# Performance work log

Measured on AMD Instinct MI355X. Metric: run time of the kernel, lower is better.

## Reference

```python
import jax, jax.numpy as jnp
import numpy as np

FEAT = 128
N_RBF = 20
CUTOFF = 5.0
N_GRAPHS = 128
ATOMS = 64
N_ATOMS = N_GRAPHS * ATOMS  # 8192
N_EDGES = N_ATOMS * 32      # 262144


def setup_inputs() -> dict:
    key = jax.random.key(0)
    ks = jax.random.split(key, 12)
    s_j = jax.random.normal(ks[0], (N_ATOMS, FEAT), jnp.float32)
    v_j = jax.random.normal(ks[1], (N_ATOMS, FEAT, 3), jnp.float32)
    r_ij = jax.random.normal(ks[2], (N_EDGES, 3), jnp.float32) * 1.5
    nbrs = jax.random.randint(ks[3], (N_EDGES, 2), 0, N_ATOMS, dtype=jnp.int32)
    num_atoms = jnp.full((N_GRAPHS,), ATOMS, dtype=jnp.int32)
    sc = 0.05
    W1 = jax.random.normal(ks[4], (FEAT, FEAT), jnp.float32) * sc
    b1 = jnp.zeros((FEAT,), jnp.float32)
    W2 = jax.random.normal(ks[5], (FEAT, 3 * FEAT), jnp.float32) * sc
    b2 = jnp.zeros((3 * FEAT,), jnp.float32)
    Wr = jax.random.normal(ks[6], (N_RBF, 3 * FEAT), jnp.float32) * sc
    br = jnp.zeros((3 * FEAT,), jnp.float32)
    Wd = jax.random.normal(ks[7], (FEAT, 3 * FEAT), jnp.float32) * sc
    bd = jnp.zeros((3 * FEAT,), jnp.float32)
    return {"s_j": s_j, "v_j": v_j, "r_ij": r_ij, "nbrs": nbrs,
            "num_atoms": num_atoms, "W1": W1, "b1": b1, "W2": W2, "b2": b2,
            "Wr": Wr, "br": br, "Wd": Wd, "bd": bd}


def _forward(s_j, v_j, r_ij, nbrs, W1, b1, W2, b2, Wr, br, Wd, bd):
    # preprocess_r
    dist = jnp.linalg.norm(r_ij, axis=-1)            # [E]
    unit = r_ij / dist[:, None]                      # [E,3]

    # InvariantMessage: per-atom MLP, gather at nbrs[:,1], times radial filter
    phi = jax.nn.silu(s_j @ W1 + b1) @ W2 + b2       # [N, 3F]
    phi_e = phi[nbrs[:, 1]]                          # [E, 3F]
    n = jnp.arange(1, N_RBF + 1, dtype=jnp.float32)
    rbf = jnp.sin(n[None, :] * jnp.pi * dist[:, None] / CUTOFF) / dist[:, None]  # [E, n_rbf]
    env = jnp.where(dist < CUTOFF, 0.5 * (jnp.cos(jnp.pi * dist / CUTOFF) + 1.0), 0.0)
    w_s = (rbf @ Wr + br) * env[:, None]             # [E, 3F]
    inv_out = (phi_e * w_s).reshape(-1, 3, FEAT)     # [E, 3, F]

    split_0 = inv_out[:, 0, :][..., None]            # [E, F, 1]
    split_1 = inv_out[:, 1, :]                       # [E, F]
    split_2 = inv_out[:, 2, :][..., None]            # [E, F, 1]

    unit_add = split_2 * unit[:, None, :]            # [E, F, 3]
    delta_v_ij = unit_add + split_0 * v_j[nbrs[:, 1]]  # [E, F, 3]
    delta_s_ij = split_1                             # [E, F]

    seg = nbrs[:, 0]
    delta_v_i = jax.ops.segment_sum(delta_v_ij, seg, num_segments=N_ATOMS)
    delta_s_l = jax.ops.segment_sum(delta_s_ij, seg, num_segments=N_ATOMS)

    # NonLocalInteraction: per-graph exact softmax attention (uniform graph size)
    qkv = s_j @ Wd + bd                              # [N, 3F]
    Q, K, V = jnp.split(qkv, 3, axis=-1)
    Qb = Q.reshape(N_GRAPHS, ATOMS, FEAT)
    Kb = K.reshape(N_GRAPHS, ATOMS, FEAT)
    Vb = V.reshape(N_GRAPHS, ATOMS, FEAT)
    scores = jnp.einsum('bqf,bkf->bqk', Qb, Kb) / jnp.sqrt(jnp.float32(FEAT))
    att = jnp.einsum('bqk,bkf->bqf', jax.nn.softmax(scores, axis=-1), Vb)
    delta_s_nl = att.reshape(N_ATOMS, FEAT)

    delta_s_i = delta_s_l + delta_s_nl
    return delta_s_i, delta_v_i


def reference(s_j, v_j, r_ij, nbrs, num_atoms, W1, b1, W2, b2, Wr, br, Wd, bd):
    # num_atoms is uniform (ATOMS per graph); attention is batched accordingly.
    return _forward(s_j, v_j, r_ij, nbrs, W1, b1, W2, b2, Wr, br, Wd, bd)
```

## Files before the change

### kernel.cpp

```cpp
#include <hip/hip_runtime.h>
#include <hip/hip_bf16.h>
#include <cstdint>

#define FEAT    128
#define NRBF    20
#define NATOMS  8192
#define NEDGES  262144
#define NGRAPH  128
#define APG     64
#define PI_F    3.14159265358979323846f
#define CUTOFF_F 5.0f
#define QTUS    ((size_t)NATOMS * 32 * 6)

typedef unsigned int uint_t;
typedef unsigned short ushort_t;
typedef __attribute__((ext_vector_type(4))) float f32x4;
typedef __attribute__((ext_vector_type(4))) short short4v;
typedef __attribute__((ext_vector_type(8))) short short8;
struct U3 { uint_t x, y, z; };

__device__ __forceinline__ float bflo(uint_t u) { return __uint_as_float(u << 16); }
__device__ __forceinline__ float bfhi(uint_t u) { return __uint_as_float(u & 0xffff0000u); }
__device__ __forceinline__ float bfus(ushort_t u) { return __uint_as_float((uint_t)u << 16); }
__device__ __forceinline__ ushort_t f2bf(float f) {
  uint_t u = __float_as_uint(f);
  return (ushort_t)((u + 0x7fffu + ((u >> 16) & 1u)) >> 16);
}
__device__ __forceinline__ uint_t pack2(float lo, float hi) {
  return (uint_t)f2bf(lo) | ((uint_t)f2bf(hi) << 16);
}

__device__ __forceinline__ ushort_t swz_elem(const float* __restrict__ W, int N,
                                             int NT, int i) {
  int jj = i & 7, lane = (i >> 3) & 63, tile = i >> 9;
  int ks = tile / NT, ctg = tile - ks * NT;
  int g = lane >> 4, q = lane & 15;
  int k = 32 * ks + 4 * g + (jj & 3) + 16 * (jj >> 2);
  int c = 16 * ctg + q;
  return f2bf(W[(size_t)k * N + c]);
}

__global__ void prep_kernel(const float* __restrict__ v_j, const float* __restrict__ W1,
                            const float* __restrict__ W2, const float* __restrict__ Wd,
                            const float* __restrict__ Wr, const float* __restrict__ br,
                            ushort_t* __restrict__ PV, ushort_t* __restrict__ w1s,
                            ushort_t* __restrict__ w2s, ushort_t* __restrict__ wds,
                            ushort_t* __restrict__ wrs) {
  int i = blockIdx.x * 256 + threadIdx.x;
  if (i < NATOMS * FEAT) {
    int j = i >> 7, f = i & 127;
    int tbl = f >> 5, fl = f & 31;
    const float* vp = v_j + (size_t)i * 3;
    uint_t* o = reinterpret_cast<uint_t*>(PV + (size_t)tbl * QTUS + ((size_t)j * 32 + fl) * 6);
    o[0] = 0u;
    o[1] = pack2(0.f, vp[0]);
    o[2] = pack2(vp[1], vp[2]);
    return;
  }
  i -= NATOMS * FEAT;
  if (i < 16384) { w1s[i] = swz_elem(W1, 128, 8, i); return; }
  i -= 16384;
  if (i < 49152) { w2s[i] = swz_elem(W2, 384, 24, i); return; }
  i -= 49152;
  if (i < 49152) { wds[i] = swz_elem(Wd, 384, 24, i); return; }
  i -= 49152;
  if (i < 12288) {
    int jj = i & 7, lane = (i >> 3) & 63, ct = i >> 9;
    int g = lane >> 4, q = lane & 15;
    int k = 4 * g + (jj & 3) + 16 * (jj >> 2);
    int f = 16 * ct + q;
    float v = (k < NRBF) ? Wr[k * 384 + f] : (k == NRBF ? br[f] : 0.f);
    wrs[i] = f2bf(v);
  }
}

__global__ __launch_bounds__(256) void gemm_mfma(
    const void* __restrict__ Asrc, int a_f32, const ushort_t* __restrict__ Wswz,
    const float* __restrict__ bias, int N, int NT, int silu, int omode,
    void* __restrict__ p0, void* __restrict__ p1) {
  __shared__ ushort_t As[64][136];
  const int t = threadIdx.x;
  const int r0 = blockIdx.x * 64, c0 = blockIdx.y * 64;
  const int w = t >> 6, l = t & 63, g = l >> 4, q = l & 15;

  short8 bf[4][4];
  #pragma unroll
  for (int ks = 0; ks < 4; ++ks)
    #pragma unroll
    for (int ct = 0; ct < 4; ++ct)
      bf[ks][ct] = *reinterpret_cast<const short8*>(
          Wswz + ((size_t)(ks * NT + (c0 >> 4) + ct) * 64 + l) * 8);

  if (a_f32) {
    const float* Af = (const float*)Asrc;
    for (int i = t; i < 64 * 32; i += 256) {
      int r = i >> 5, k4 = i & 31;
      float4 v = *reinterpret_cast<const float4*>(Af + (size_t)(r0 + r) * 128 + 4 * k4);
      ushort4 o = {f2bf(v.x), f2bf(v.y), f2bf(v.z), f2bf(v.w)};
      *reinterpret_cast<ushort4*>(&As[r][4 * k4]) = o;
    }
  } else {
    const ushort_t* Ab = (const ushort_t*)Asrc;
    for (int i = t; i < 64 * 16; i += 256) {
      int r = i >> 4, g8 = i & 15;
      short8 v = *reinterpret_cast<const short8*>(Ab + (size_t)(r0 + r) * 128 + 8 * g8);
      *reinterpret_cast<short8*>(&As[r][8 * g8]) = v;
    }
  }
  __syncthreads();

  f32x4 acc[4] = {};
  #pragma unroll
  for (int ks = 0; ks < 4; ++ks) {
    const ushort_t* ap = &As[16 * w + q][32 * ks + 4 * g];
    short4v alo = *reinterpret_cast<const short4v*>(ap);
    short4v ahi = *reinterpret_cast<const short4v*>(ap + 16);
    short8 af;
    af[0] = alo[0]; af[1] = alo[1]; af[2] = alo[2]; af[3] = alo[3];
    af[4] = ahi[0]; af[5] = ahi[1]; af[6] = ahi[2]; af[7] = ahi[3];
    #pragma unroll
    for (int ct = 0; ct < 4; ++ct)
      acc[ct] = __builtin_amdgcn_mfma_f32_16x16x32_bf16(af, bf[ks][ct], acc[ct], 0, 0, 0);
  }

  #pragma unroll
  for (int ct = 0; ct < 4; ++ct) {
    int col = c0 + 16 * ct + q;
    float bb = bias[col];
    #pragma unroll
    for (int r = 0; r < 4; ++r) {
      float o = acc[ct][r] + bb;
      if (silu) o = o / (1.f + __expf(-o));
      int row = r0 + 16 * w + 4 * g + r;
      if (omode == 1) {
        ((ushort_t*)p0)[(size_t)row * N + col] = f2bf(o);
      } else if (omode == 2) {
        int f = col & 127, s = col >> 7;
        int tbl = f >> 5, fl = f & 31;
        ((ushort_t*)p0)[(size_t)tbl * QTUS + ((size_t)row * 32 + fl) * 6 + s] = f2bf(o);
      } else {
        if (col < 128) ((float*)p0)[(size_t)row * 128 + col] = o;
        else           ((ushort_t*)p1)[(size_t)row * 256 + col - 128] = f2bf(o);
      }
    }
  }
}

__global__ void hist_kernel(const int* __restrict__ nbrs, int* __restrict__ counts) {
  int e = blockIdx.x * blockDim.x + threadIdx.x;
  if (e < NEDGES) atomicAdd(&counts[nbrs[2 * e]], 1);
}

__global__ __launch_bounds__(1024) void scan_kernel(
    const int* __restrict__ counts, int* __restrict__ offs, int* __restrict__ cursor) {
  __shared__ int part[1024];
  const int t = threadIdx.x;
  int local[8];
  int s = 0;
  #pragma unroll
  for (int i = 0; i < 8; ++i) { local[i] = counts[t * 8 + i]; s += local[i]; }
  part[t] = s;
  __syncthreads();
  for (int off = 1; off < 1024; off <<= 1) {
    int v = part[t];
    int add = (t >= off) ? part[t - off] : 0;
    __syncthreads();
    part[t] = v + add;
    __syncthreads();
  }
  int excl = part[t] - s;
  #pragma unroll
  for (int i = 0; i < 8; ++i) {
    offs[t * 8 + i] = excl;
    cursor[t * 8 + i] = excl;
    excl += local[i];
  }
  if (t == 1023) offs[NATOMS] = excl;
}

__global__ void scatter_kernel(const int* __restrict__ nbrs, const float* __restrict__ r_ij,
                               int* __restrict__ cursor, uint4* __restrict__ erec) {
  int e = blockIdx.x * blockDim.x + threadIdx.x;
  if (e < NEDGES) {
    int2 nb = *reinterpret_cast<const int2*>(nbrs + 2 * e);
    int pos = atomicAdd(&cursor[nb.x], 1);
    const float* rp = r_ij + 3 * e;
    erec[pos] = make_uint4((uint_t)nb.y, __float_as_uint(rp[0]),
                           __float_as_uint(rp[1]), __float_as_uint(rp[2]));
  }
}

__global__ __launch_bounds__(256) void edge_mfma7(
    const uint4* __restrict__ erec, const int* __restrict__ offs,
    const ushort_t* __restrict__ PV, const ushort_t* __restrict__ wrs,
    float* __restrict__ out_s, float* __restrict__ out_v) {
  __shared__ short8 sW[6 * 64];
  const int t = threadIdx.x;
  const int qtr = blockIdx.x & 3;
  for (int i = t; i < 6 * 64; i += 256) {
    int tl = i >> 6, l2 = i & 63;
    int s = tl >> 1, c = tl & 1;
    sW[i] = *reinterpret_cast<const short8*>(
        wrs + ((size_t)(s * 8 + 2 * qtr + c) * 64 + l2) * 8);
  }
  __syncthreads();

  const int w = t >> 6, l = t & 63, g = l >> 4, q = l & 15;
  const int atom = (blockIdx.x >> 2) * 4 + w;
  const int start = offs[atom], end = offs[atom + 1];
  const float c1 = PI_F / CUTOFF_F;
  const char* PVb = reinterpret_cast<const char*>(PV) + (size_t)qtr * QTUS * 2;

  float ds[2] = {};
  float dv[2][3] = {};

  uint4 er = make_uint4(0u, 0u, 0u, 0u);
  if (start + q < end) er = erec[start + q];

  for (int eb = start; eb < end; eb += 16) {
    uint4 ern = make_uint4(0u, 0u, 0u, 0u);
    if (eb + 16 + q < end) ern = erec[eb + 16 + q];
    float ang = 0.f, ie = 0.f, env = 0.f, u0 = 0.f, u1 = 0.f, u2 = 0.f;
    int jn = 0;
    if (eb + q < end) {
      jn = (int)er.x;
      float x = __uint_as_float(er.y), y = __uint_as_float(er.z), z = __uint_as_float(er.w);
      float d = sqrtf(x * x + y * y + z * z);
      float inv = 1.f / d;
      ang = c1 * d;
      env = (d < CUTOFF_F) ? 0.5f * (__cosf(ang) + 1.f) : 0.f;
      ie = inv * env;
      u0 = x * inv; u1 = y * inv; u2 = z * inv;
    }
    const char* pb[4];
    float ub[4][3];
    #pragma unroll
    for (int r = 0; r < 4; ++r) {
      int src = 4 * g + r;
      int jr = __shfl(jn, src, 64);
      ub[r][0] = __shfl(u0, src, 64);
      ub[r][1] = __shfl(u1, src, 64);
      ub[r][2] = __shfl(u2, src, 64);
      pb[r] = PVb + (size_t)jr * 384 + (size_t)q * 12;
    }
    U3 ld[2][4];
    #pragma unroll
    for (int c = 0; c < 2; ++c)
      #pragma unroll
      for (int r = 0; r < 4; ++r)
        ld[c][r] = *reinterpret_cast<const U3*>(pb[r] + (size_t)c * 192);
    short8 af;
    #pragma unroll
    for (int jj = 0; jj < 8; ++jj) {
      int k = 4 * g + (jj & 3) + 16 * (jj >> 2);
      float v = (k < NRBF) ? ie * __sinf((float)(k + 1) * ang)
                           : (k == NRBF ? env : 0.f);
      af[jj] = (short)f2bf(v);
    }
    #pragma unroll
    for (int c = 0; c < 2; ++c) {
      short8 b0 = sW[(0 * 2 + c) * 64 + l];
      short8 b1 = sW[(1 * 2 + c) * 64 + l];
      short8 b2 = sW[(2 * 2 + c) * 64 + l];
      f32x4 z4 = {0.f, 0.f, 0.f, 0.f};
      f32x4 cs0 = __builtin_amdgcn_mfma_f32_16x16x32_bf16(af, b0, z4, 0, 0, 0);
      f32x4 cs1 = __builtin_amdgcn_mfma_f32_16x16x32_bf16(af, b1, z4, 0, 0, 0);
      f32x4 cs2 = __builtin_amdgcn_mfma_f32_16x16x32_bf16(af, b2, z4, 0, 0, 0);
      #pragma unroll
      for (int r = 0; r < 4; ++r) {
        U3 u = ld[c][r];
        float p0 = bflo(u.x), p1 = bfhi(u.x);
        float p2 = bflo(u.y), v0 = bfhi(u.y);
        float v1 = bflo(u.z), v2 = bfhi(u.z);
        float pw0 = p0 * cs0[r];
        ds[c] += p1 * cs1[r];
        float pw2 = p2 * cs2[r];
        dv[c][0] += pw0 * v0 + pw2 * ub[r][0];
        dv[c][1] += pw0 * v1 + pw2 * ub[r][1];
        dv[c][2] += pw0 * v2 + pw2 * ub[r][2];
      }
    }
    er = ern;
  }

  #pragma unroll
  for (int c = 0; c < 2; ++c) {
    float x = ds[c];
    x += __shfl_xor(x, 16, 64); x += __shfl_xor(x, 32, 64);
    ds[c] = x;
    #pragma unroll
    for (int cc = 0; cc < 3; ++cc) {
      float y = dv[c][cc];
      y += __shfl_xor(y, 16, 64); y += __shfl_xor(y, 32, 64);
      dv[c][cc] = y;
    }
  }
  if (g < 2) {
    float sv = (g == 0) ? ds[0] : ds[1];
    float d0 = (g == 0) ? dv[0][0] : dv[1][0];
    float d1 = (g == 0) ? dv[0][1] : dv[1][1];
    float d2 = (g == 0) ? dv[0][2] : dv[1][2];
    int f = 32 * qtr + 16 * g + q;
    out_s[(size_t)atom * FEAT + f] = sv;
    float* ov = out_v + (size_t)atom * 384 + (size_t)f * 3;
    ov[0] = d0; ov[1] = d1; ov[2] = d2;
  }
}

__device__ __forceinline__ float wave_max64(float v) {
  #pragma unroll
  for (int m = 32; m > 0; m >>= 1) v = fmaxf(v, __shfl_xor(v, m, 64));
  return v;
}
__device__ __forceinline__ float wave_sum64(float v) {
  #pragma unroll
  for (int m = 32; m > 0; m >>= 1) v += __shfl_xor(v, m, 64);
  return v;
}

__global__ __launch_bounds__(256) void attn_kernel(const float* __restrict__ Qf,
                                                   const ushort_t* __restrict__ kvbf,
                                                   float* __restrict__ out_s) {
  __shared__ float4 Ks4[64 * 32];
  __shared__ float  Vs[64][130];
  __shared__ float  Ps[4][4][64];
  const int b = blockIdx.x >> 1, half = blockIdx.x & 1;
  const int t = threadIdx.x;
  const float* qbase = Qf + (size_t)b * APG * 128;
  const ushort_t* kvb = kvbf + (size_t)b * APG * 256;

  for (int i = t; i < 64 * 32; i += 256) {
    int a = i >> 5, gg = i & 31;
    ushort4 k4 = *reinterpret_cast<const ushort4*>(kvb + a * 256 + 4 * gg);
    float4 kf = {bfus(k4.x), bfus(k4.y), bfus(k4.z), bfus(k4.w)};
    Ks4[a * 32 + (gg ^ (a & 7))] = kf;
  }
  for (int i = t; i < 64 * 32; i += 256) {
    int a = i >> 5, gg = i & 31;
    ushort4 v4 = *reinterpret_cast<const ushort4*>(kvb + a * 256 + 128 + 4 * gg);
    Vs[a][4 * gg + 0] = bfus(v4.x); Vs[a][4 * gg + 1] = bfus(v4.y);
    Vs[a][4 * gg + 2] = bfus(v4.z); Vs[a][4 * gg + 3] = bfus(v4.w);
  }
  __syncthreads();

  const int w = t >> 6, l = t & 63;
  const float scale = 0.08838834764831845f;

  for (int qq = 8 * half + w; qq < 8 * half + 8; qq += 4) {
    const float* q0p = qbase + (size_t)(4 * qq + 0) * 128;
    const float* q1p = qbase + (size_t)(4 * qq + 1) * 128;
    const float* q2p = qbase + (size_t)(4 * qq + 2) * 128;
    const float* q3p = qbase + (size_t)(4 * qq + 3) * 128;
    float s0 = 0.f, s1 = 0.f, s2 = 0.f, s3 = 0.f;
    #pragma unroll 8
    for (int i = 0; i < 32; ++i) {
      float4 k = Ks4[l * 32 + (i ^ (l & 7))];
      float4 q0 = *reinterpret_cast<const float4*>(q0p + 4 * i);
      float4 q1 = *reinterpret_cast<const float4*>(q1p + 4 * i);
      float4 q2 = *reinterpret_cast<const float4*>(q2p + 4 * i);
      float4 q3 = *reinterpret_cast<const float4*>(q3p + 4 * i);
      s0 += q0.x * k.x + q0.y * k.y + q0.z * k.z + q0.w * k.w;
      s1 += q1.x * k.x + q1.y * k.y + q1.z * k.z + q1.w * k.w;
      s2 += q2.x * k.x + q2.y * k.y + q2.z * k.z + q2.w * k.w;
      s3 += q3.x * k.x + q3.y * k.y + q3.z * k.z + q3.w * k.w;
    }
    s0 *= scale; s1 *= scale; s2 *= scale; s3 *= scale;

    float p0 = __expf(s0 - wave_max64(s0));
    float p1 = __expf(s1 - wave_max64(s1));
    float p2 = __expf(s2 - wave_max64(s2));
    float p3 = __expf(s3 - wave_max64(s3));
    p0 /= wave_sum64(p0); p1 /= wave_sum64(p1);
    p2 /= wave_sum64(p2); p3 /= wave_sum64(p3);

    Ps[w][0][l] = p0; Ps[w][1][l] = p1; Ps[w][2][l] = p2; Ps[w][3][l] = p3;
    __threadfence_block();

    float a00 = 0.f, a01 = 0.f, a10 = 0.f, a11 = 0.f;
    float a20 = 0.f, a21 = 0.f, a30 = 0.f, a31 = 0.f;
    for (int a = 0; a < 64; ++a) {
      float2 v = *reinterpret_cast<const float2*>(&Vs[a][2 * l]);
      float pa0 = Ps[w][0][a], pa1 = Ps[w][1][a];
      float pa2 = Ps[w][2][a], pa3 = Ps[w][3][a];
      a00 += pa0 * v.x; a01 += pa0 * v.y;
      a10 += pa1 * v.x; a11 += pa1 * v.y;
      a20 += pa2 * v.x; a21 += pa2 * v.y;
      a30 += pa3 * v.x; a31 += pa3 * v.y;
    }
    size_t row0 = (size_t)(b * APG + 4 * qq) * FEAT + 2 * l;
    float2* o0 = reinterpret_cast<float2*>(out_s + row0);
    float2* o1 = reinterpret_cast<float2*>(out_s + row0 + FEAT);
    float2* o2 = reinterpret_cast<float2*>(out_s + row0 + 2 * FEAT);
    float2* o3 = reinterpret_cast<float2*>(out_s + row0 + 3 * FEAT);
    float2 c0 = *o0; c0.x += a00; c0.y += a01; *o0 = c0;
    float2 c1 = *o1; c1.x += a10; c1.y += a11; *o1 = c1;
    float2 c2 = *o2; c2.x += a20; c2.y += a21; *o2 = c2;
    float2 c3 = *o3; c3.x += a30; c3.y += a31; *o3 = c3;
    __threadfence_block();
  }
}

extern "C" void kernel_launch(void* const* d_in, const int* in_sizes, int n_in,
                              void* d_out, int out_size, void* d_ws, size_t ws_size,
                              hipStream_t stream) {
  const float* s_j  = (const float*)d_in[0];
  const float* v_j  = (const float*)d_in[1];
  const float* r_ij = (const float*)d_in[2];
  const int*   nbrs = (const int*)d_in[3];
  const float* W1   = (const float*)d_in[5];
  const float* b1   = (const float*)d_in[6];
  const float* W2   = (const float*)d_in[7];
  const float* b2   = (const float*)d_in[8];
  const float* Wr   = (const float*)d_in[9];
  const float* br   = (const float*)d_in[10];
  const float* Wd   = (const float*)d_in[11];
  const float* bd   = (const float*)d_in[12];

  float* out_s = (float*)d_out;
  float* out_v = out_s + (size_t)NATOMS * FEAT;

  float*    Qf   = (float*)d_ws;
  ushort_t* kvbf = (ushort_t*)(Qf + NATOMS * FEAT);
  ushort_t* PV   = kvbf + (size_t)NATOMS * 256;
  ushort_t* w1s  = PV + 4 * QTUS;
  ushort_t* w2s  = w1s + 16384;
  ushort_t* wds  = w2s + 49152;
  ushort_t* wrs  = wds + 49152;
  ushort_t* h_bf = wrs + 12288;
  uint4*    erec = (uint4*)h_bf;
  int* offs   = (int*)((char*)h_bf + 4194304);
  int* cursor = offs + (NATOMS + 1);
  int* counts = cursor + NATOMS;

  int prep_total = NATOMS * FEAT + 16384 + 49152 + 49152 + 12288;
  prep_kernel<<<(prep_total + 255) / 256, 256, 0, stream>>>(
      v_j, W1, W2, Wd, Wr, br, PV, w1s, w2s, wds, wrs);

  gemm_mfma<<<dim3(NATOMS / 64, 2), 256, 0, stream>>>(
      s_j, 1, w1s, b1, 128, 8, 1, 1, h_bf, nullptr);
  gemm_mfma<<<dim3(NATOMS / 64, 6), 256, 0, stream>>>(
      h_bf, 0, w2s, b2, 384, 24, 0, 2, PV, nullptr);

  hipMemsetAsync(counts, 0, NATOMS * sizeof(int), stream);
  hist_kernel<<<NEDGES / 256, 256, 0, stream>>>(nbrs, counts);
  scan_kernel<<<1, 1024, 0, stream>>>(counts, offs, cursor);
  scatter_kernel<<<NEDGES / 256, 256, 0, stream>>>(nbrs, r_ij, cursor, erec);

  gemm_mfma<<<dim3(NATOMS / 64, 6), 256, 0, stream>>>(
      s_j, 1, wds, bd, 384, 24, 0, 3, Qf, kvbf);

  edge_mfma7<<<NATOMS, 256, 0, stream>>>(erec, offs, PV, wrs, out_s, out_v);
  attn_kernel<<<NGRAPH * 2, 256, 0, stream>>>(Qf, kvbf, out_s);
}
```

Measured before the change: 146.6 us.

## Fuse MLP GEMMs and process several atoms per wave in edge kernel

Two per-atom MLP GEMMs are merged into one kernel that keeps the SiLU hidden activations in shared memory, so the bf16 intermediate buffer and one launch go away. The edge kernel now has each wave walk APW consecutive atoms, prefetching the next edge records across atom boundaries. This cuts block count and the repeated shared-memory load of radial weights. The risks are fewer blocks (less parallelism and latency hiding) and serialised work per wave.

```diff
diff --git a/kernel.cpp b/kernel.cpp
--- a/kernel.cpp
+++ b/kernel.cpp
@@ -11,6 +11,7 @@
 #define PI_F    3.14159265358979323846f
 #define CUTOFF_F 5.0f
 #define QTUS    ((size_t)NATOMS * 32 * 6)
+#define APW     8
 
 typedef unsigned int uint_t;
 typedef unsigned short ushort_t;
@@ -74,6 +75,83 @@
   }
 }
 
+__global__ __launch_bounds__(256) void gemm_fused12(
+    const float* __restrict__ s_j, const ushort_t* __restrict__ w1s,
+    const float* __restrict__ b1, const ushort_t* __restrict__ w2s,
+    const float* __restrict__ b2, ushort_t* __restrict__ PV) {
+  __shared__ ushort_t As[64][136];
+  __shared__ ushort_t Hs[64][136];
+  const int t = threadIdx.x;
+  const int r0 = blockIdx.x * 64;
+  const int w = t >> 6, l = t & 63, g = l >> 4, q = l & 15;
+
+  for (int i = t; i < 64 * 32; i += 256) {
+    int r = i >> 5, k4 = i & 31;
+    float4 v = *reinterpret_cast<const float4*>(s_j + (size_t)(r0 + r) * 128 + 4 * k4);
+    ushort4 o = {f2bf(v.x), f2bf(v.y), f2bf(v.z), f2bf(v.w)};
+    *reinterpret_cast<ushort4*>(&As[r][4 * k4]) = o;
+  }
+  __syncthreads();
+
+  short8 afr[4];
+  #pragma unroll
+  for (int ks = 0; ks < 4; ++ks) {
+    const ushort_t* ap = &As[16 * w + q][32 * ks + 4 * g];
+    short4v alo = *reinterpret_cast<const short4v*>(ap);
+    short4v ahi = *reinterpret_cast<const short4v*>(ap + 16);
+    afr[ks] = short8{alo[0], alo[1], alo[2], alo[3], ahi[0], ahi[1], ahi[2], ahi[3]};
+  }
+  #pragma unroll
+  for (int ct = 0; ct < 8; ++ct) {
+    f32x4 acc = {};
+    #pragma unroll
+    for (int ks = 0; ks < 4; ++ks) {
+      short8 bf = *reinterpret_cast<const short8*>(
+          w1s + ((size_t)(ks * 8 + ct) * 64 + l) * 8);
+      acc = __builtin_amdgcn_mfma_f32_16x16x32_bf16(afr[ks], bf, acc, 0, 0, 0);
+    }
+    float bb = b1[16 * ct + q];
+    #pragma unroll
+    for (int r = 0; r < 4; ++r) {
+      float o = acc[r] + bb;
+      o = o / (1.f + __expf(-o));
+      Hs[16 * w + 4 * g + r][16 * ct + q] = f2bf(o);
+    }
+  }
+  __syncthreads();
+
+  short8 hfr[4];
+  #pragma unroll
+  for (int ks = 0; ks < 4; ++ks) {
+    const ushort_t* ap = &Hs[16 * w + q][32 * ks + 4 * g];
+    short4v alo = *reinterpret_cast<const short4v*>(ap);
+    short4v ahi = *reinterpret_cast<const short4v*>(ap + 16);
+    hfr[ks] = short8{alo[0], alo[1], alo[2], alo[3], ahi[0], ahi[1], ahi[2], ahi[3]};
+  }
+  for (int cb = 0; cb < 6; ++cb) {
+    #pragma unroll
+    for (int ct = 0; ct < 4; ++ct) {
+      f32x4 acc = {};
+      #pragma unroll
+      for (int ks = 0; ks < 4; ++ks) {
+        short8 bf = *reinterpret_cast<const short8*>(
+            w2s + ((size_t)(ks * 24 + cb * 4 + ct) * 64 + l) * 8);
+        acc = __builtin_amdgcn_mfma_f32_16x16x32_bf16(hfr[ks], bf, acc, 0, 0, 0);
+      }
+      int col = cb * 64 + 16 * ct + q;
+      float bb = b2[col];
+      int f = col & 127, s = col >> 7;
+      int tbl = f >> 5, fl = f & 31;
+      #pragma unroll
+      for (int r = 0; r < 4; ++r) {
+        float o = acc[r] + bb;
+        int row = r0 + 16 * w + 4 * g + r;
+        PV[(size_t)tbl * QTUS + ((size_t)row * 32 + fl) * 6 + s] = f2bf(o);
+      }
+    }
+  }
+}
+
 __global__ __launch_bounds__(256) void gemm_mfma(
     const void* __restrict__ Asrc, int a_f32, const ushort_t* __restrict__ Wswz,
     const float* __restrict__ bias, int N, int NT, int silu, int omode,
@@ -134,10 +212,6 @@
       int row = r0 + 16 * w + 4 * g + r;
       if (omode == 1) {
         ((ushort_t*)p0)[(size_t)row * N + col] = f2bf(o);
-      } else if (omode == 2) {
-        int f = col & 127, s = col >> 7;
-        int tbl = f >> 5, fl = f & 31;
-        ((ushort_t*)p0)[(size_t)tbl * QTUS + ((size_t)row * 32 + fl) * 6 + s] = f2bf(o);
       } else {
         if (col < 128) ((float*)p0)[(size_t)row * 128 + col] = o;
         else           ((ushort_t*)p1)[(size_t)row * 256 + col - 128] = f2bf(o);
@@ -190,7 +264,7 @@
   }
 }
 
-__global__ __launch_bounds__(256) void edge_mfma7(
+__global__ __launch_bounds__(256) void edge_mfma8(
     const uint4* __restrict__ erec, const int* __restrict__ offs,
     const ushort_t* __restrict__ PV, const ushort_t* __restrict__ wrs,
     float* __restrict__ out_s, float* __restrict__ out_v) {
@@ -206,104 +280,116 @@
   __syncthreads();
 
   const int w = t >> 6, l = t & 63, g = l >> 4, q = l & 15;
-  const int atom = (blockIdx.x >> 2) * 4 + w;
-  const int start = offs[atom], end = offs[atom + 1];
+  const int a0 = ((blockIdx.x >> 2) * 4 + w) * APW;
   const float c1 = PI_F / CUTOFF_F;
   const char* PVb = reinterpret_cast<const char*>(PV) + (size_t)qtr * QTUS * 2;
 
-  float ds[2] = {};
-  float dv[2][3] = {};
-
+  int eb = offs[a0];
+  int end = offs[a0 + 1];
   uint4 er = make_uint4(0u, 0u, 0u, 0u);
-  if (start + q < end) er = erec[start + q];
-
-  for (int eb = start; eb < end; eb += 16) {
-    uint4 ern = make_uint4(0u, 0u, 0u, 0u);
-    if (eb + 16 + q < end) ern = erec[eb + 16 + q];
-    float ang = 0.f, ie = 0.f, env = 0.f, u0 = 0.f, u1 = 0.f, u2 = 0.f;
-    int jn = 0;
-    if (eb + q < end) {
-      jn = (int)er.x;
-      float x = __uint_as_float(er.y), y = __uint_as_float(er.z), z = __uint_as_float(er.w);
-      float d = sqrtf(x * x + y * y + z * z);
-      float inv = 1.f / d;
-      ang = c1 * d;
-      env = (d < CUTOFF_F) ? 0.5f * (__cosf(ang) + 1.f) : 0.f;
-      ie = inv * env;
-      u0 = x * inv; u1 = y * inv; u2 = z * inv;
-    }
-    const char* pb[4];
-    float ub[4][3];
-    #pragma unroll
-    for (int r = 0; r < 4; ++r) {
-      int src = 4 * g + r;
-      int jr = __shfl(jn, src, 64);
-      ub[r][0] = __shfl(u0, src, 64);
-      ub[r][1] = __shfl(u1, src, 64);
-      ub[r][2] = __shfl(u2, src, 64);
-      pb[r] = PVb + (size_t)jr * 384 + (size_t)q * 12;
-    }
-    U3 ld[2][4];
+  if (eb + q < end) er = erec[eb + q];
+
+  for (int aidx = 0; aidx < APW; ++aidx) {
+    const int end_next = (aidx + 1 < APW) ? offs[a0 + aidx + 2] : 0;
+    float ds0 = 0.f, ds1 = 0.f;
+    float dv[2][3] = {};
+
+    for (;;) {
+      const bool last = (eb + 16 >= end);
+      const int neb = last ? end : (eb + 16);
+      const int nend = last ? ((aidx + 1 < APW) ? end_next : neb) : end;
+      uint4 ern = make_uint4(0u, 0u, 0u, 0u);
+      if (neb + q < nend) ern = erec[neb + q];
+
+      float ang = 0.f, ie = 0.f, env = 0.f, u0 = 0.f, u1 = 0.f, u2 = 0.f;
+      int jn = 0;
+      if (eb + q < end) {
+        jn = (int)er.x;
+        float x = __uint_as_float(er.y), y = __uint_as_float(er.z), z = __uint_as_float(er.w);
+        float d = sqrtf(x * x + y * y + z * z);
+        float inv = 1.f / d;
+        ang = c1 * d;
+        env = (d < CUTOFF_F) ? 0.5f * (__cosf(ang) + 1.f) : 0.f;
+        ie = inv * env;
+        u0 = x * inv; u1 = y * inv; u2 = z * inv;
+      }
+      const char* pb[4];
+      float ub[4][3];
+      #pragma unroll
+      for (int r = 0; r < 4; ++r) {
+        int src = 4 * g + r;
+        int jr = __shfl(jn, src, 64);
+        ub[r][0] = __shfl(u0, src, 64);
+        ub[r][1] = __shfl(u1, src, 64);
+        ub[r][2] = __shfl(u2, src, 64);
+        pb[r] = PVb + (size_t)jr * 384 + (size_t)q * 12;
+      }
+      U3 ld[2][4];
+      #pragma unroll
+      for (int c = 0; c < 2; ++c)
+        #pragma unroll
+        for (int r = 0; r < 4; ++r)
+          ld[c][r] = *reinterpret_cast<const U3*>(pb[r] + (size_t)c * 192);
+      short8 af;
+      #pragma unroll
+      for (int jj = 0; jj < 8; ++jj) {
+        int k = 4 * g + (jj & 3) + 16 * (jj >> 2);
+        float v = (k < NRBF) ? ie * __sinf((float)(k + 1) * ang)
+                             : (k == NRBF ? env : 0.f);
+        af[jj] = (short)f2bf(v);
+      }
+      #pragma unroll
+      for (int c = 0; c < 2; ++c) {
+        short8 b0 = sW[(0 * 2 + c) * 64 + l];
+        short8 b1 = sW[(1 * 2 + c) * 64 + l];
+        short8 b2 = sW[(2 * 2 + c) * 64 + l];
+        f32x4 z4 = {0.f, 0.f, 0.f, 0.f};
+        f32x4 cs0 = __builtin_amdgcn_mfma_f32_16x16x32_bf16(af, b0, z4, 0, 0, 0);
+        f32x4 cs1 = __builtin_amdgcn_mfma_f32_16x16x32_bf16(af, b1, z4, 0, 0, 0);
+        f32x4 cs2 = __builtin_amdgcn_mfma_f32_16x16x32_bf16(af, b2, z4, 0, 0, 0);
+        #pragma unroll
+        for (int r = 0; r < 4; ++r) {
+          U3 u = ld[c][r];
+          float p0 = bflo(u.x), p1 = bfhi(u.x);
+          float p2 = bflo(u.y), v0 = bfhi(u.y);
+          float v1 = bflo(u.z), v2 = bfhi(u.z);
+          float pw0 = p0 * cs0[r];
+          if (c == 0) ds0 += p1 * cs1[r]; else ds1 += p1 * cs1[r];
+          float pw2 = p2 * cs2[r];
+          dv[c][0] += pw0 * v0 + pw2 * ub[r][0];
+          dv[c][1] += pw0 * v1 + pw2 * ub[r][1];
+          dv[c][2] += pw0 * v2 + pw2 * ub[r][2];
+        }
+      }
+      er = ern;
+      eb = neb;
+      if (last) break;
+    }
+
+    float r0v = ds0, r1v = ds1;
+    r0v += __shfl_xor(r0v, 16, 64); r0v += __shfl_xor(r0v, 32, 64);
+    r1v += __shfl_xor(r1v, 16, 64); r1v += __shfl_xor(r1v, 32, 64);
+    float dvr[2][3];
     #pragma unroll
     for (int c = 0; c < 2; ++c)
       #pragma unroll
-      for (int r = 0; r < 4; ++r)
-        ld[c][r] = *reinterpret_cast<const U3*>(pb[r] + (size_t)c * 192);
-    short8 af;
-    #pragma unroll
-    for (int jj = 0; jj < 8; ++jj) {
-      int k = 4 * g + (jj & 3) + 16 * (jj >> 2);
-      float v = (k < NRBF) ? ie * __sinf((float)(k + 1) * ang)
-                           : (k == NRBF ? env : 0.f);
-      af[jj] = (short)f2bf(v);
-    }
-    #pragma unroll
-    for (int c = 0; c < 2; ++c) {
-      short8 b0 = sW[(0 * 2 + c) * 64 + l];
-      short8 b1 = sW[(1 * 2 + c) * 64 + l];
-      short8 b2 = sW[(2 * 2 + c) * 64 + l];
-      f32x4 z4 = {0.f, 0.f, 0.f, 0.f};
-      f32x4 cs0 = __builtin_amdgcn_mfma_f32_16x16x32_bf16(af, b0, z4, 0, 0, 0);
-      f32x4 cs1 = __builtin_amdgcn_mfma_f32_16x16x32_bf16(af, b1, z4, 0, 0, 0);
-      f32x4 cs2 = __builtin_amdgcn_mfma_f32_16x16x32_bf16(af, b2, z4, 0, 0, 0);
-      #pragma unroll
-      for (int r = 0; r < 4; ++r) {
-        U3 u = ld[c][r];
-        float p0 = bflo(u.x), p1 = bfhi(u.x);
-        float p2 = bflo(u.y), v0 = bfhi(u.y);
-        float v1 = bflo(u.z), v2 = bfhi(u.z);
-        float pw0 = p0 * cs0[r];
-        ds[c] += p1 * cs1[r];
-        float pw2 = p2 * cs2[r];
-        dv[c][0] += pw0 * v0 + pw2 * ub[r][0];
-        dv[c][1] += pw0 * v1 + pw2 * ub[r][1];
-        dv[c][2] += pw0 * v2 + pw2 * ub[r][2];
-      }
-    }
-    er = ern;
-  }
-
-  #pragma unroll
-  for (int c = 0; c < 2; ++c) {
-    float x = ds[c];
-    x += __shfl_xor(x, 16, 64); x += __shfl_xor(x, 32, 64);
-    ds[c] = x;
-    #pragma unroll
-    for (int cc = 0; cc < 3; ++cc) {
-      float y = dv[c][cc];
-      y += __shfl_xor(y, 16, 64); y += __shfl_xor(y, 32, 64);
-      dv[c][cc] = y;
-    }
-  }
-  if (g < 2) {
-    float sv = (g == 0) ? ds[0] : ds[1];
-    float d0 = (g == 0) ? dv[0][0] : dv[1][0];
-    float d1 = (g == 0) ? dv[0][1] : dv[1][1];
-    float d2 = (g == 0) ? dv[0][2] : dv[1][2];
-    int f = 32 * qtr + 16 * g + q;
-    out_s[(size_t)atom * FEAT + f] = sv;
-    float* ov = out_v + (size_t)atom * 384 + (size_t)f * 3;
-    ov[0] = d0; ov[1] = d1; ov[2] = d2;
+      for (int cc = 0; cc < 3; ++cc) {
+        float y = dv[c][cc];
+        y += __shfl_xor(y, 16, 64); y += __shfl_xor(y, 32, 64);
+        dvr[c][cc] = y;
+      }
+    if (g < 2) {
+      int atom = a0 + aidx;
+      float sv = (g == 0) ? r0v : r1v;
+      float d0 = (g == 0) ? dvr[0][0] : dvr[1][0];
+      float d1 = (g == 0) ? dvr[0][1] : dvr[1][1];
+      float d2 = (g == 0) ? dvr[0][2] : dvr[1][2];
+      int f = 32 * qtr + 16 * g + q;
+      out_s[(size_t)atom * FEAT + f] = sv;
+      float* ov = out_v + (size_t)atom * 384 + (size_t)f * 3;
+      ov[0] = d0; ov[1] = d1; ov[2] = d2;
+    }
+    end = end_next;
   }
 }
 
@@ -426,9 +512,8 @@
   ushort_t* w2s  = w1s + 16384;
   ushort_t* wds  = w2s + 49152;
   ushort_t* wrs  = wds + 49152;
-  ushort_t* h_bf = wrs + 12288;
-  uint4*    erec = (uint4*)h_bf;
-  int* offs   = (int*)((char*)h_bf + 4194304);
+  uint4*    erec = (uint4*)(wrs + 12288);
+  int* offs   = (int*)(erec + NEDGES);
   int* cursor = offs + (NATOMS + 1);
   int* counts = cursor + NATOMS;
 
@@ -436,10 +521,7 @@
   prep_kernel<<<(prep_total + 255) / 256, 256, 0, stream>>>(
       v_j, W1, W2, Wd, Wr, br, PV, w1s, w2s, wds, wrs);
 
-  gemm_mfma<<<dim3(NATOMS / 64, 2), 256, 0, stream>>>(
-      s_j, 1, w1s, b1, 128, 8, 1, 1, h_bf, nullptr);
-  gemm_mfma<<<dim3(NATOMS / 64, 6), 256, 0, stream>>>(
-      h_bf, 0, w2s, b2, 384, 24, 0, 2, PV, nullptr);
+  gemm_fused12<<<NATOMS / 64, 256, 0, stream>>>(s_j, w1s, b1, w2s, b2, PV);
 
   hipMemsetAsync(counts, 0, NATOMS * sizeof(int), stream);
   hist_kernel<<<NEDGES / 256, 256, 0, stream>>>(nbrs, counts);
@@ -449,6 +531,6 @@
   gemm_mfma<<<dim3(NATOMS / 64, 6), 256, 0, stream>>>(
       s_j, 1, wds, bd, 384, 24, 0, 3, Qf, kvbf);
 
-  edge_mfma7<<<NATOMS, 256, 0, stream>>>(erec, offs, PV, wrs, out_s, out_v);
+  edge_mfma8<<<NATOMS / APW, 256, 0, stream>>>(erec, offs, PV, wrs, out_s, out_v);
   attn_kernel<<<NGRAPH * 2, 256, 0, stream>>>(Qf, kvbf, out_s);
 }
```

Result: faster. 141.5 us (-3.5%).
